# Kernel tuning notes

Measured on AMD Instinct MI355X. Metric: run time of the kernel, lower is better.

Reference implementation:

```python
import jax, jax.numpy as jnp
import numpy as np

B, S, D, H = 2, 2048, 1024, 16
DH = D // H

def setup_inputs() -> dict:
    key = jax.random.key(0)
    ks = jax.random.split(key, 8)
    scale = 0.02
    return {
        'query': jax.random.normal(ks[0], (B, S, D), jnp.float32),
        'key': jax.random.normal(ks[1], (B, S, D), jnp.float32),
        'value': jax.random.normal(ks[2], (B, S, D), jnp.float32),
        'mask': jax.random.randint(ks[3], (B, 1, 1, S), 0, 2).astype(jnp.float32),
        'Wq': jax.random.normal(ks[4], (D, D), jnp.float32) * scale,
        'bq': jnp.zeros((D,), jnp.float32),
        'Wk': jax.random.normal(ks[5], (D, D), jnp.float32) * scale,
        'bk': jnp.zeros((D,), jnp.float32),
        'Wv': jax.random.normal(ks[6], (D, D), jnp.float32) * scale,
        'bv': jnp.zeros((D,), jnp.float32),
        'Wo': jax.random.normal(ks[7], (D, D), jnp.float32) * scale,
        'bo': jnp.zeros((D,), jnp.float32),
    }

def _split_heads(x):
    # [B, S, D] -> [B, H, S, DH]
    b, s, _ = x.shape
    return x.reshape(b, s, H, DH).transpose(0, 2, 1, 3)

def reference(query, key, value, mask, Wq, bq, Wk, bk, Wv, bv, Wo, bo):
    q = _split_heads(query @ Wq + bq)
    k = _split_heads(key @ Wk + bk)
    v = _split_heads(value @ Wv + bv)
    logits = jnp.einsum('bhqd,bhkd->bhqk', q, k) / jnp.sqrt(jnp.float32(DH))
    logits = logits + mask * (-1e9)  # mask==1 means masked out
    attn = jax.nn.softmax(logits, axis=-1)
    out = jnp.einsum('bhqk,bhkd->bhqd', attn, v)  # [B,H,S,DH]
    out = out.transpose(0, 2, 1, 3).reshape(query.shape[0], -1, D)
    return out @ Wo + bo
```

## Files before the change

### kernel.cpp

```cpp
#include <hip/hip_runtime.h>
#include <hip/hip_bf16.h>
#include <stdint.h>

using short8  = __attribute__((ext_vector_type(8))) short;
using f32x4   = __attribute__((ext_vector_type(4))) float;
using f32x16  = __attribute__((ext_vector_type(16))) float;

__device__ inline unsigned short f2bf(float f) {
    union { float f; unsigned int u; } v; v.f = f;
    unsigned int u = v.u;
    unsigned int r = (u + 0x7FFFu + ((u >> 16) & 1u)) >> 16;
    return (unsigned short)r;
}

__device__ inline unsigned short bfu(float f) {
    __hip_bfloat16 h = __float2bfloat16(f);
    union { __hip_bfloat16 h; unsigned short u; } c; c.h = h;
    return c.u;
}

__device__ inline float bf2f(unsigned short u) {
    union { unsigned int u; float f; } v; v.u = (unsigned int)u << 16;
    return v.f;
}

__device__ inline unsigned int bfpk(float lo, float hi) {
    return (unsigned int)bfu(lo) | ((unsigned int)bfu(hi) << 16);
}

__device__ inline f32x4 mfma16(short8 a, short8 b, f32x4 c) {
    return __builtin_amdgcn_mfma_f32_16x16x32_bf16(a, b, c, 0, 0, 0);
}
__device__ inline f32x16 mfma32(short8 a, short8 b, f32x16 c) {
    return __builtin_amdgcn_mfma_f32_32x32x16_bf16(a, b, c, 0, 0, 0);
}

__device__ inline void gld16(const void* g, void* l) {
    __builtin_amdgcn_global_load_lds(
        (const __attribute__((address_space(1))) unsigned int*)g,
        (__attribute__((address_space(3))) unsigned int*)l, 16, 0, 0);
}

#define SEQ 2048
#define DIM 1024
#define NH  16
#define DH  64
#define MROWS 4096
#define OHALF 4194304
#define LHALF 65536

__global__ __launch_bounds__(256) void wcvt_kernel(
    const float* __restrict__ W0, const float* __restrict__ W1,
    const float* __restrict__ W2, const float* __restrict__ W3,
    unsigned short* __restrict__ Wt)
{
    __shared__ unsigned short tile[64][72];
    const float* W = (blockIdx.y == 0) ? W0 : (blockIdx.y == 1) ? W1
                   : (blockIdx.y == 2) ? W2 : W3;
    unsigned short* out = Wt + (size_t)blockIdx.y * DIM * DIM;
    const int t  = threadIdx.x;
    const int tk = blockIdx.x >> 4, tn = blockIdx.x & 15;
    const int k0 = tk * 64, n0 = tn * 64;

    #pragma unroll
    for (int j = 0; j < 4; ++j) {
        int c = t + j * 256;
        int r = c >> 4, c4 = c & 15;
        float4 v = *(const float4*)(W + (size_t)(k0 + r) * DIM + n0 + c4 * 4);
        tile[c4 * 4 + 0][r] = f2bf(v.x);
        tile[c4 * 4 + 1][r] = f2bf(v.y);
        tile[c4 * 4 + 2][r] = f2bf(v.z);
        tile[c4 * 4 + 3][r] = f2bf(v.w);
    }
    __syncthreads();
    #pragma unroll
    for (int j = 0; j < 2; ++j) {
        int c = t + j * 256;
        int r = c >> 3, c8 = c & 7;
        *(short8*)(out + (size_t)(n0 + r) * DIM + k0 + c8 * 8) =
            *(const short8*)&tile[r][c8 * 8];
    }
}

__global__ __launch_bounds__(256) void xcvt_kernel(
    const float* __restrict__ Xq, const float* __restrict__ Xk,
    const float* __restrict__ Xv, unsigned short* __restrict__ Xbf)
{
    const int zz = blockIdx.y;
    const float* src = (zz == 0) ? Xq : (zz == 1) ? Xk : Xv;
    size_t i8 = ((size_t)blockIdx.x * 256 + threadIdx.x) * 8;
    float4 v0 = *(const float4*)(src + i8);
    float4 v1 = *(const float4*)(src + i8 + 4);
    union { unsigned int u[4]; short8 s8; } p;
    p.u[0] = bfpk(v0.x, v0.y); p.u[1] = bfpk(v0.z, v0.w);
    p.u[2] = bfpk(v1.x, v1.y); p.u[3] = bfpk(v1.z, v1.w);
    *(short8*)(Xbf + (size_t)zz * MROWS * DIM + i8) = p.s8;
}

template<bool BF16A>
__global__ __launch_bounds__(256, 3) void proj_kernel(
    const unsigned short* __restrict__ Xbf,
    const float* __restrict__ Xq, const float* __restrict__ Xk, const float* __restrict__ Xv,
    const unsigned short* __restrict__ Wt,
    const float* __restrict__ bq, const float* __restrict__ bk, const float* __restrict__ bv,
    const float* __restrict__ maskp,
    unsigned short* __restrict__ Qh, unsigned short* __restrict__ Kh,
    unsigned short* __restrict__ Vt)
{
    __shared__ unsigned short Al[128][64];
    __shared__ unsigned short Bl[128][64];

    const int bid = blockIdx.x;
    const int z = bid >> 8;
    const int p = bid & 255;
    const int qq = p >> 3;
    const int mb = (p & 7) | ((qq & 3) << 3);
    const int nb = qq >> 2;
    const int m0 = mb * 128, n0 = nb * 128;

    const unsigned short* W = Wt + (size_t)z * DIM * DIM;
    const float* bias = (z == 0) ? bq : (z == 1) ? bk : bv;

    const int t = threadIdx.x, lane = t & 63, w = t >> 6;
    const int l16 = lane & 15, hi = lane >> 4;
    const int wm = w >> 1, wn = w & 1;
    const int row2 = t >> 1, part = t & 1;
    const int swz = (row2 & 7) << 3;
    const int cb = part * 32;

    const unsigned short* Asrc_bf = nullptr;
    const float* Asrc_f = nullptr;
    if constexpr (BF16A) {
        Asrc_bf = Xbf + (size_t)z * MROWS * DIM + (size_t)(m0 + row2) * DIM + cb;
    } else {
        const float* X = (z == 0) ? Xq : (z == 1) ? Xk : Xv;
        Asrc_f = X + (size_t)(m0 + row2) * DIM + cb;
    }
    const unsigned short* Bsrc = W + (size_t)(n0 + row2) * DIM + cb;

    f32x4 zero4 = {0.f, 0.f, 0.f, 0.f};
    f32x4 acc[4][4];
    #pragma unroll
    for (int i = 0; i < 4; ++i)
        #pragma unroll
        for (int j = 0; j < 4; ++j) acc[i][j] = zero4;

    short8 na[4], nbv[4];
    #pragma unroll
    for (int i = 0; i < 4; ++i) {
        if constexpr (BF16A) {
            na[i] = *(const short8*)(Asrc_bf + i * 8);
        } else {
            float4 f0 = *(const float4*)(Asrc_f + i * 8);
            float4 f1 = *(const float4*)(Asrc_f + i * 8 + 4);
            union { unsigned int u[4]; short8 s8; } pk;
            pk.u[0] = bfpk(f0.x, f0.y); pk.u[1] = bfpk(f0.z, f0.w);
            pk.u[2] = bfpk(f1.x, f1.y); pk.u[3] = bfpk(f1.z, f1.w);
            na[i] = pk.s8;
        }
        nbv[i] = *(const short8*)(Bsrc + i * 8);
    }
    #pragma unroll
    for (int i = 0; i < 4; ++i) {
        *(short8*)&Al[row2][(cb + i * 8) ^ swz] = na[i];
        *(short8*)&Bl[row2][(cb + i * 8) ^ swz] = nbv[i];
    }
    __syncthreads();

    for (int kt = 0; kt < DIM / 64; ++kt) {
        if (kt < DIM / 64 - 1) {
            const int k0n = (kt + 1) * 64;
            #pragma unroll
            for (int i = 0; i < 4; ++i) {
                if constexpr (BF16A) {
                    na[i] = *(const short8*)(Asrc_bf + k0n + i * 8);
                } else {
                    float4 f0 = *(const float4*)(Asrc_f + k0n + i * 8);
                    float4 f1 = *(const float4*)(Asrc_f + k0n + i * 8 + 4);
                    union { unsigned int u[4]; short8 s8; } pk;
                    pk.u[0] = bfpk(f0.x, f0.y); pk.u[1] = bfpk(f0.z, f0.w);
                    pk.u[2] = bfpk(f1.x, f1.y); pk.u[3] = bfpk(f1.z, f1.w);
                    na[i] = pk.s8;
                }
                nbv[i] = *(const short8*)(Bsrc + k0n + i * 8);
            }
        }
        #pragma unroll
        for (int kc = 0; kc < 2; ++kc) {
            short8 af[4], bfv[4];
            #pragma unroll
            for (int i = 0; i < 4; ++i) {
                int ra = wm * 64 + i * 16 + l16;
                af[i] = *(const short8*)&Al[ra][(kc * 32 + hi * 8) ^ ((ra & 7) << 3)];
            }
            #pragma unroll
            for (int j = 0; j < 4; ++j) {
                int rb = wn * 64 + j * 16 + l16;
                bfv[j] = *(const short8*)&Bl[rb][(kc * 32 + hi * 8) ^ ((rb & 7) << 3)];
            }
            #pragma unroll
            for (int i = 0; i < 4; ++i)
                #pragma unroll
                for (int j = 0; j < 4; ++j)
                    acc[i][j] = mfma16(af[i], bfv[j], acc[i][j]);
        }
        __syncthreads();
        if (kt < DIM / 64 - 1) {
            #pragma unroll
            for (int i = 0; i < 4; ++i) {
                *(short8*)&Al[row2][(cb + i * 8) ^ swz] = na[i];
                *(short8*)&Bl[row2][(cb + i * 8) ^ swz] = nbv[i];
            }
        }
        __syncthreads();
    }

    float bj[4];
    #pragma unroll
    for (int j = 0; j < 4; ++j) bj[j] = bias[n0 + wn * 64 + j * 16 + l16];

    if (z == 2) {
        #pragma unroll
        for (int i = 0; i < 4; ++i) {
            int mrow0 = m0 + wm * 64 + i * 16 + hi * 4;
            int bb = mrow0 >> 11, s = mrow0 & (SEQ - 1);
            float4 mv = *(const float4*)(maskp + (size_t)bb * SEQ + s);
            float w0 = 1.f - mv.x, w1 = 1.f - mv.y, w2 = 1.f - mv.z, w3 = 1.f - mv.w;
            #pragma unroll
            for (int j = 0; j < 4; ++j) {
                int n = n0 + wn * 64 + j * 16 + l16;
                int dn = n & 63, hh = n >> 6;
                ushort4 pk;
                pk.x = bfu((acc[i][j][0] + bj[j]) * w0);
                pk.y = bfu((acc[i][j][1] + bj[j]) * w1);
                pk.z = bfu((acc[i][j][2] + bj[j]) * w2);
                pk.w = bfu((acc[i][j][3] + bj[j]) * w3);
                int scol = (s & ~31) | ((((s >> 3) & 3) ^ ((dn >> 1) & 3)) << 3) | (s & 7);
                *(ushort4*)(Vt + ((size_t)(bb * NH + hh) * DH + dn) * SEQ + scol) = pk;
            }
        }
    } else if (z == 1) {
        #pragma unroll
        for (int i = 0; i < 4; ++i) {
            #pragma unroll
            for (int j = 0; j < 4; ++j) {
                int n = n0 + wn * 64 + j * 16 + l16;
                int hh = n >> 6, d = n & 63;
                #pragma unroll
                for (int r = 0; r < 4; ++r) {
                    int mrow = m0 + wm * 64 + i * 16 + hi * 4 + r;
                    int bb = mrow >> 11, s = mrow & (SEQ - 1);
                    int dsw = (d & 7) | ((((d >> 3) ^ (s & 7)) & 7) << 3);
                    Kh[((size_t)(bb * NH + hh) * SEQ + s) * DH + dsw] =
                        bfu(acc[i][j][r] + bj[j]);
                }
            }
        }
    } else {
        const float sc = 0.125f * 1.4426950408889634f;
        #pragma unroll
        for (int i = 0; i < 4; ++i) {
            #pragma unroll
            for (int j = 0; j < 4; ++j) {
                int n = n0 + wn * 64 + j * 16 + l16;
                int hh = n >> 6, d = n & 63;
                #pragma unroll
                for (int r = 0; r < 4; ++r) {
                    int mrow = m0 + wm * 64 + i * 16 + hi * 4 + r;
                    int bb = mrow >> 11, s = mrow & (SEQ - 1);
                    Qh[((size_t)(bb * NH + hh) * SEQ + s) * DH + d] =
                        bfu((acc[i][j][r] + bj[j]) * sc);
                }
            }
        }
    }
}

template<bool SPLIT>
__global__ __launch_bounds__(512) void attn_kernel(
    const unsigned short* __restrict__ Qh,
    const unsigned short* __restrict__ Kh,
    const unsigned short* __restrict__ Vtp,
    const float* __restrict__ mask,
    unsigned short* __restrict__ AO,
    unsigned short* __restrict__ Opart,
    float* __restrict__ lpart)
{
    constexpr int NT = SPLIT ? 32 : 64;
    __shared__ unsigned short Kl[2][32 * 64];
    __shared__ unsigned short Vl[2][64 * 32];
    __shared__ unsigned short Ml[2048];

    const int t = threadIdx.x, lane = t & 63, w = t >> 6;
    const int l31 = lane & 31, h32 = lane >> 5;
    const int bh = blockIdx.x, b = bh >> 4, h = bh & (NH - 1);
    const int q0 = blockIdx.y * 256 + w * 32;
    const int half = SPLIT ? blockIdx.z : 0;
    const int tile0 = half * NT;

    const unsigned short* Q = Qh + (size_t)bh * SEQ * DH;
    const unsigned short* K = Kh + (size_t)bh * SEQ * DH;
    const unsigned short* V = Vtp + (size_t)bh * DH * SEQ;

    const int cs = (w & 3) * 64 + lane;
    const bool isK = (w < 4);

    short8 qf[4];
    #pragma unroll
    for (int ds = 0; ds < 4; ++ds)
        qf[ds] = *(const short8*)(Q + (size_t)(q0 + l31) * DH + ds * 16 + h32 * 8);

    f32x16 o[2], ol;
    #pragma unroll
    for (int r = 0; r < 16; ++r) { o[0][r] = 0.f; o[1][r] = 0.f; ol[r] = 0.f; }

    {
        const int kb0 = tile0 * 32;
        if (isK) gld16(K + (size_t)(kb0 + (cs >> 3)) * DH + (cs & 7) * 8, &Kl[0][cs * 8]);
        else     gld16(V + (size_t)(cs >> 2) * SEQ + kb0 + (cs & 3) * 8,  &Vl[0][cs * 8]);
        const float* mb = mask + (size_t)b * SEQ + t * 4;
        float4 m = *(const float4*)mb;
        unsigned int pm0 = bfpk(1.f - m.x, 1.f - m.y);
        unsigned int pm1 = bfpk(1.f - m.z, 1.f - m.w);
        *(unsigned int*)&Ml[t * 4]     = pm0;
        *(unsigned int*)&Ml[t * 4 + 2] = pm1;
    }
    asm volatile("s_waitcnt vmcnt(0)" ::: "memory");
    __syncthreads();

    for (int it = 0; it < NT; ++it) {
        const int tile = tile0 + it;
        const int cur = it & 1;
        const int kb = tile * 32;
        const int nkb = ((tile + 1) & 63) * 32;

        if (isK) gld16(K + (size_t)(nkb + (cs >> 3)) * DH + (cs & 7) * 8, &Kl[cur ^ 1][cs * 8]);
        else     gld16(V + (size_t)(cs >> 2) * SEQ + nkb + (cs & 3) * 8,  &Vl[cur ^ 1][cs * 8]);

        short8 wf[2];
        #pragma unroll
        for (int ss = 0; ss < 2; ++ss)
            wf[ss] = *(const short8*)&Ml[kb + ss * 16 + h32 * 8];

        f32x16 st;
        #pragma unroll
        for (int r = 0; r < 16; ++r) st[r] = 0.f;
        __builtin_amdgcn_s_setprio(1);
        #pragma unroll
        for (int ds = 0; ds < 4; ++ds) {
            short8 kfr = *(const short8*)
                &Kl[cur][l31 * 64 + (((ds * 2 + h32) ^ (l31 & 7)) * 8)];
            st = mfma32(kfr, qf[ds], st);
        }
        __builtin_amdgcn_s_setprio(0);

        #pragma unroll
        for (int r = 0; r < 16; ++r) st[r] = exp2f(st[r]);

        short8 pa[2];
        #pragma unroll
        for (int ss = 0; ss < 2; ++ss) {
            const int rb = ss * 8;
            unsigned int a0 = bfpk(st[rb + 0], st[rb + 1]);
            unsigned int a1 = bfpk(st[rb + 2], st[rb + 3]);
            unsigned int b0 = bfpk(st[rb + 4], st[rb + 5]);
            unsigned int b1 = bfpk(st[rb + 6], st[rb + 7]);
            asm volatile("v_permlane32_swap_b32 %0, %1" : "+v"(a0), "+v"(b0));
            asm volatile("v_permlane32_swap_b32 %0, %1" : "+v"(a1), "+v"(b1));
            union { unsigned int u[4]; short8 s8; } up;
            up.u[0] = a0; up.u[1] = a1; up.u[2] = b0; up.u[3] = b1;
            pa[ss] = up.s8;
        }

        __builtin_amdgcn_s_setprio(1);
        #pragma unroll
        for (int ss = 0; ss < 2; ++ss) {
            #pragma unroll
            for (int dblk = 0; dblk < 2; ++dblk) {
                int vrow = dblk * 32 + l31;
                short8 vfr = *(const short8*)
                    &Vl[cur][vrow * 32 + (((ss * 2 + h32) ^ ((l31 >> 1) & 3)) * 8)];
                o[dblk] = mfma32(pa[ss], vfr, o[dblk]);
            }
            ol = mfma32(pa[ss], wf[ss], ol);
        }
        __builtin_amdgcn_s_setprio(0);

        asm volatile("s_waitcnt vmcnt(0)" ::: "memory");
        __syncthreads();
    }

    if constexpr (SPLIT) {
        #pragma unroll
        for (int dblk = 0; dblk < 2; ++dblk) {
            #pragma unroll
            for (int r = 0; r < 16; ++r) {
                int q = (r & 3) + 8 * (r >> 2) + 4 * h32;
                Opart[(size_t)half * OHALF + (size_t)(b * SEQ + q0 + q) * DIM
                      + h * DH + dblk * 32 + l31] = bfu(o[dblk][r]);
            }
        }
        if (l31 == 0) {
            #pragma unroll
            for (int r = 0; r < 16; ++r) {
                int q = (r & 3) + 8 * (r >> 2) + 4 * h32;
                lpart[(size_t)half * LHALF + bh * SEQ + q0 + q] = ol[r];
            }
        }
    } else {
        float rcl[16];
        #pragma unroll
        for (int r = 0; r < 16; ++r) rcl[r] = 1.0f / ol[r];
        #pragma unroll
        for (int dblk = 0; dblk < 2; ++dblk) {
            #pragma unroll
            for (int r = 0; r < 16; ++r) {
                int q = (r & 3) + 8 * (r >> 2) + 4 * h32;
                AO[(size_t)(b * SEQ + q0 + q) * DIM + h * DH + dblk * 32 + l31] =
                    bfu(o[dblk][r] * rcl[r]);
            }
        }
    }
}

template<bool SPLIT>
__global__ __launch_bounds__(256, 3) void outproj_kernel(
    const unsigned short* __restrict__ Op0, const float* __restrict__ lpart,
    const unsigned short* __restrict__ W,
    const float* __restrict__ bias, float* __restrict__ Out)
{
    __shared__ unsigned short Al[128][64];
    __shared__ unsigned short Bl[64][64];

    const int p = blockIdx.x;
    const int qq = p >> 3;
    const int mb = (p & 7) | ((qq & 3) << 3);
    const int nb = qq >> 2;
    const int m0 = mb * 128, n0 = nb * 64;

    const int t = threadIdx.x, lane = t & 63, w = t >> 6;
    const int l16 = lane & 15, hi = lane >> 4;
    const int wm = w >> 1, wn = w & 1;
    const int row2 = t >> 1, part = t & 1;
    const int swzA = (row2 & 7) << 3;
    const int cb = part * 32;
    const int row4 = t >> 2, part4 = t & 3;
    const int swzB = (row4 & 7) << 3;
    const int cb4 = part4 * 16;

    const int arow = m0 + row2;
    const int bb = arow >> 11, sA = arow & (SEQ - 1);
    const unsigned short* Asrc = Op0 + (size_t)arow * DIM + cb;
    const unsigned short* Bsrc = W + (size_t)(n0 + row4) * DIM + cb4;

    f32x4 zero4 = {0.f, 0.f, 0.f, 0.f};
    f32x4 acc[4][2];
    #pragma unroll
    for (int i = 0; i < 4; ++i) { acc[i][0] = zero4; acc[i][1] = zero4; }

    short8 o0[4], o1[4], nbv[2];
    float rlv = 0.f;

    auto load_kt = [&](int kt) {
        const int k0 = kt * 64;
        if constexpr (SPLIT) {
            size_t li = (size_t)(bb * NH + kt) * SEQ + sA;
            rlv = 1.0f / (lpart[li] + lpart[(size_t)LHALF + li]);
            #pragma unroll
            for (int i = 0; i < 4; ++i) {
                o0[i] = *(const short8*)(Asrc + k0 + i * 8);
                o1[i] = *(const short8*)(Asrc + (size_t)OHALF + k0 + i * 8);
            }
        } else {
            #pragma unroll
            for (int i = 0; i < 4; ++i)
                o0[i] = *(const short8*)(Asrc + k0 + i * 8);
        }
        #pragma unroll
        for (int c = 0; c < 2; ++c)
            nbv[c] = *(const short8*)(Bsrc + k0 + c * 8);
    };
    auto stage = [&]() {
        #pragma unroll
        for (int i = 0; i < 4; ++i) {
            short8 na;
            if constexpr (SPLIT) {
                union { unsigned int u[4]; short8 s8; } pk;
                #pragma unroll
                for (int j = 0; j < 4; ++j) {
                    float f0 = (bf2f((unsigned short)o0[i][2*j])   + bf2f((unsigned short)o1[i][2*j]))   * rlv;
                    float f1 = (bf2f((unsigned short)o0[i][2*j+1]) + bf2f((unsigned short)o1[i][2*j+1])) * rlv;
                    pk.u[j] = bfpk(f0, f1);
                }
                na = pk.s8;
            } else {
                na = o0[i];
            }
            *(short8*)&Al[row2][(cb + i * 8) ^ swzA] = na;
        }
        #pragma unroll
        for (int c = 0; c < 2; ++c)
            *(short8*)&Bl[row4][(cb4 + c * 8) ^ swzB] = nbv[c];
    };

    load_kt(0);
    stage();
    __syncthreads();

    for (int kt = 0; kt < DIM / 64; ++kt) {
        if (kt < DIM / 64 - 1) load_kt(kt + 1);
        #pragma unroll
        for (int kc = 0; kc < 2; ++kc) {
            short8 af[4], bfv[2];
            #pragma unroll
            for (int i = 0; i < 4; ++i) {
                int ra = wm * 64 + i * 16 + l16;
                af[i] = *(const short8*)&Al[ra][(kc * 32 + hi * 8) ^ ((ra & 7) << 3)];
            }
            #pragma unroll
            for (int j = 0; j < 2; ++j) {
                int rb = wn * 32 + j * 16 + l16;
                bfv[j] = *(const short8*)&Bl[rb][(kc * 32 + hi * 8) ^ ((rb & 7) << 3)];
            }
            #pragma unroll
            for (int i = 0; i < 4; ++i)
                #pragma unroll
                for (int j = 0; j < 2; ++j)
                    acc[i][j] = mfma16(af[i], bfv[j], acc[i][j]);
        }
        __syncthreads();
        if (kt < DIM / 64 - 1) {
            stage();
        }
        __syncthreads();
    }

    float bj[2];
    #pragma unroll
    for (int j = 0; j < 2; ++j) bj[j] = bias[n0 + wn * 32 + j * 16 + l16];
    #pragma unroll
    for (int i = 0; i < 4; ++i) {
        #pragma unroll
        for (int j = 0; j < 2; ++j) {
            int n = n0 + wn * 32 + j * 16 + l16;
            #pragma unroll
            for (int r = 0; r < 4; ++r) {
                int m = m0 + wm * 64 + i * 16 + hi * 4 + r;
                Out[(size_t)m * DIM + n] = acc[i][j][r] + bj[j];
            }
        }
    }
}

extern "C" void kernel_launch(void* const* d_in, const int* in_sizes, int n_in,
                              void* d_out, int out_size, void* d_ws, size_t ws_size,
                              hipStream_t stream) {
    const float* query = (const float*)d_in[0];
    const float* key   = (const float*)d_in[1];
    const float* value = (const float*)d_in[2];
    const float* mask  = (const float*)d_in[3];
    const float* Wq    = (const float*)d_in[4];
    const float* bq    = (const float*)d_in[5];
    const float* Wk    = (const float*)d_in[6];
    const float* bk    = (const float*)d_in[7];
    const float* Wv    = (const float*)d_in[8];
    const float* bv    = (const float*)d_in[9];
    const float* Wo    = (const float*)d_in[10];
    const float* bo    = (const float*)d_in[11];
    float* out = (float*)d_out;

    char* ws = (char*)d_ws;
    unsigned short* Wt    = (unsigned short*)(ws);
    unsigned short* Qh    = (unsigned short*)(ws + (size_t)8  * 1024 * 1024);
    unsigned short* Kh    = (unsigned short*)(ws + (size_t)16 * 1024 * 1024);
    unsigned short* Vt    = (unsigned short*)(ws + (size_t)24 * 1024 * 1024);
    unsigned short* Opart = (unsigned short*)(ws + (size_t)32 * 1024 * 1024);
    float*          lpart = (float*)         (ws + (size_t)48 * 1024 * 1024);
    unsigned short* Xbf   = (unsigned short*)(ws + (size_t)32 * 1024 * 1024);
    const unsigned short* WtO = Wt + (size_t)3 * 1024 * 1024;

    wcvt_kernel<<<dim3(256, 4), 256, 0, stream>>>(Wq, Wk, Wv, Wo, Wt);
    if (ws_size >= (size_t)56 * 1024 * 1024) {
        xcvt_kernel<<<dim3(2048, 3), 256, 0, stream>>>(query, key, value, Xbf);
        proj_kernel<true><<<768, 256, 0, stream>>>(Xbf, query, key, value, Wt,
                                                   bq, bk, bv, mask, Qh, Kh, Vt);
        attn_kernel<true><<<dim3(32, 8, 2), 512, 0, stream>>>(Qh, Kh, Vt, mask,
                                                              nullptr, Opart, lpart);
        outproj_kernel<true><<<512, 256, 0, stream>>>(Opart, lpart, WtO, bo, out);
    } else {
        proj_kernel<false><<<768, 256, 0, stream>>>(nullptr, query, key, value, Wt,
                                                    bq, bk, bv, mask, Qh, Kh, Vt);
        attn_kernel<false><<<dim3(32, 8, 1), 512, 0, stream>>>(Qh, Kh, Vt, mask,
                                                               Opart, nullptr, nullptr);
        outproj_kernel<false><<<512, 256, 0, stream>>>(Opart, nullptr, WtO, bo, out);
    }
}
```

Measured before the change: 144.7 us.

## Compact unmasked keys/values so attention only iterates over valid key tiles

```diff
diff --git a/kernel.cpp b/kernel.cpp
--- a/kernel.cpp
+++ b/kernel.cpp
@@ -80,6 +80,48 @@
         *(short8*)(out + (size_t)(n0 + r) * DIM + k0 + c8 * 8) =
             *(const short8*)&tile[r][c8 * 8];
     }
+}
+
+__global__ __launch_bounds__(256) void mask_scan_kernel(
+    const float* __restrict__ mask, int* __restrict__ pos, int* __restrict__ cnt)
+{
+    __shared__ int sums[256];
+    const int b = blockIdx.x, t = threadIdx.x;
+    const float* m = mask + (size_t)b * SEQ;
+    int flags[8], s = 0;
+    #pragma unroll
+    for (int i = 0; i < 8; ++i) {
+        flags[i] = (m[t * 8 + i] == 0.0f) ? 1 : 0;
+        s += flags[i];
+    }
+    sums[t] = s;
+    __syncthreads();
+    if (t == 0) {
+        int acc = 0;
+        for (int i = 0; i < 256; ++i) { int x = sums[i]; sums[i] = acc; acc += x; }
+        cnt[b] = acc;
+    }
+    __syncthreads();
+    int base = sums[t];
+    #pragma unroll
+    for (int i = 0; i < 8; ++i) {
+        pos[(size_t)b * SEQ + t * 8 + i] = flags[i] ? base : -1;
+        base += flags[i];
+    }
+}
+
+__global__ __launch_bounds__(256) void pad_kernel(
+    const int* __restrict__ cnt, unsigned short* __restrict__ Kh,
+    unsigned short* __restrict__ Vt)
+{
+    const int bh = blockIdx.x, b = bh >> 4;
+    const int c = cnt[b];
+    if ((c & 31) == 0) return;
+    const int base = c & ~31;
+    const int t = threadIdx.x;
+    short8 z = {0, 0, 0, 0, 0, 0, 0, 0};
+    *(short8*)(Kh + ((size_t)bh * SEQ + base + (t >> 3)) * DH + (t & 7) * 8) = z;
+    *(short8*)(Vt + (size_t)bh * DH * SEQ + (size_t)(t >> 2) * SEQ + base + (t & 3) * 8) = z;
 }
 
 __global__ __launch_bounds__(256) void xcvt_kernel(
@@ -103,7 +145,7 @@
     const float* __restrict__ Xq, const float* __restrict__ Xk, const float* __restrict__ Xv,
     const unsigned short* __restrict__ Wt,
     const float* __restrict__ bq, const float* __restrict__ bk, const float* __restrict__ bv,
-    const float* __restrict__ maskp,
+    const int* __restrict__ pos,
     unsigned short* __restrict__ Qh, unsigned short* __restrict__ Kh,
     unsigned short* __restrict__ Vt)
 {
@@ -224,34 +266,36 @@
         for (int i = 0; i < 4; ++i) {
             int mrow0 = m0 + wm * 64 + i * 16 + hi * 4;
             int bb = mrow0 >> 11, s = mrow0 & (SEQ - 1);
-            float4 mv = *(const float4*)(maskp + (size_t)bb * SEQ + s);
-            float w0 = 1.f - mv.x, w1 = 1.f - mv.y, w2 = 1.f - mv.z, w3 = 1.f - mv.w;
-            #pragma unroll
-            for (int j = 0; j < 4; ++j) {
-                int n = n0 + wn * 64 + j * 16 + l16;
-                int dn = n & 63, hh = n >> 6;
-                ushort4 pk;
-                pk.x = bfu((acc[i][j][0] + bj[j]) * w0);
-                pk.y = bfu((acc[i][j][1] + bj[j]) * w1);
-                pk.z = bfu((acc[i][j][2] + bj[j]) * w2);
-                pk.w = bfu((acc[i][j][3] + bj[j]) * w3);
-                int scol = (s & ~31) | ((((s >> 3) & 3) ^ ((dn >> 1) & 3)) << 3) | (s & 7);
-                *(ushort4*)(Vt + ((size_t)(bb * NH + hh) * DH + dn) * SEQ + scol) = pk;
+            #pragma unroll
+            for (int r = 0; r < 4; ++r) {
+                int p_ = pos[(size_t)bb * SEQ + s + r];
+                if (p_ < 0) continue;
+                #pragma unroll
+                for (int j = 0; j < 4; ++j) {
+                    int n = n0 + wn * 64 + j * 16 + l16;
+                    int dn = n & 63, hh = n >> 6;
+                    int scol = (p_ & ~31) | ((((p_ >> 3) & 3) ^ ((dn >> 1) & 3)) << 3)
+                             | (p_ & 7);
+                    Vt[((size_t)(bb * NH + hh) * DH + dn) * SEQ + scol] =
+                        bfu(acc[i][j][r] + bj[j]);
+                }
             }
         }
     } else if (z == 1) {
         #pragma unroll
         for (int i = 0; i < 4; ++i) {
-            #pragma unroll
-            for (int j = 0; j < 4; ++j) {
-                int n = n0 + wn * 64 + j * 16 + l16;
-                int hh = n >> 6, d = n & 63;
-                #pragma unroll
-                for (int r = 0; r < 4; ++r) {
-                    int mrow = m0 + wm * 64 + i * 16 + hi * 4 + r;
-                    int bb = mrow >> 11, s = mrow & (SEQ - 1);
-                    int dsw = (d & 7) | ((((d >> 3) ^ (s & 7)) & 7) << 3);
-                    Kh[((size_t)(bb * NH + hh) * SEQ + s) * DH + dsw] =
+            int mrow0 = m0 + wm * 64 + i * 16 + hi * 4;
+            int bb = mrow0 >> 11, s = mrow0 & (SEQ - 1);
+            #pragma unroll
+            for (int r = 0; r < 4; ++r) {
+                int p_ = pos[(size_t)bb * SEQ + s + r];
+                if (p_ < 0) continue;
+                #pragma unroll
+                for (int j = 0; j < 4; ++j) {
+                    int n = n0 + wn * 64 + j * 16 + l16;
+                    int hh = n >> 6, d = n & 63;
+                    int dsw = (d & 7) | ((((d >> 3) ^ (p_ & 7)) & 7) << 3);
+                    Kh[((size_t)(bb * NH + hh) * SEQ + p_) * DH + dsw] =
                         bfu(acc[i][j][r] + bj[j]);
                 }
             }
@@ -281,22 +325,25 @@
     const unsigned short* __restrict__ Qh,
     const unsigned short* __restrict__ Kh,
     const unsigned short* __restrict__ Vtp,
-    const float* __restrict__ mask,
+    const int* __restrict__ cntbuf,
     unsigned short* __restrict__ AO,
     unsigned short* __restrict__ Opart,
     float* __restrict__ lpart)
 {
-    constexpr int NT = SPLIT ? 32 : 64;
     __shared__ unsigned short Kl[2][32 * 64];
     __shared__ unsigned short Vl[2][64 * 32];
-    __shared__ unsigned short Ml[2048];
 
     const int t = threadIdx.x, lane = t & 63, w = t >> 6;
     const int l31 = lane & 31, h32 = lane >> 5;
     const int bh = blockIdx.x, b = bh >> 4, h = bh & (NH - 1);
     const int q0 = blockIdx.y * 256 + w * 32;
     const int half = SPLIT ? blockIdx.z : 0;
-    const int tile0 = half * NT;
+
+    const int cnt = cntbuf[b];
+    const int NTt = (cnt + 31) >> 5;
+    const int NTh0 = (NTt + 1) >> 1;
+    const int t0   = (SPLIT && half) ? NTh0 : 0;
+    const int myNT = SPLIT ? (half ? NTt - NTh0 : NTh0) : NTt;
 
     const unsigned short* Q = Qh + (size_t)bh * SEQ * DH;
     const unsigned short* K = Kh + (size_t)bh * SEQ * DH;
@@ -315,32 +362,36 @@
     for (int r = 0; r < 16; ++r) { o[0][r] = 0.f; o[1][r] = 0.f; ol[r] = 0.f; }
 
     {
-        const int kb0 = tile0 * 32;
+        const int kb0 = t0 * 32;
         if (isK) gld16(K + (size_t)(kb0 + (cs >> 3)) * DH + (cs & 7) * 8, &Kl[0][cs * 8]);
         else     gld16(V + (size_t)(cs >> 2) * SEQ + kb0 + (cs & 3) * 8,  &Vl[0][cs * 8]);
-        const float* mb = mask + (size_t)b * SEQ + t * 4;
-        float4 m = *(const float4*)mb;
-        unsigned int pm0 = bfpk(1.f - m.x, 1.f - m.y);
-        unsigned int pm1 = bfpk(1.f - m.z, 1.f - m.w);
-        *(unsigned int*)&Ml[t * 4]     = pm0;
-        *(unsigned int*)&Ml[t * 4 + 2] = pm1;
     }
     asm volatile("s_waitcnt vmcnt(0)" ::: "memory");
     __syncthreads();
 
-    for (int it = 0; it < NT; ++it) {
-        const int tile = tile0 + it;
+    for (int it = 0; it < myNT; ++it) {
+        const int tile = t0 + it;
         const int cur = it & 1;
         const int kb = tile * 32;
-        const int nkb = ((tile + 1) & 63) * 32;
+        const int nt_ = (it + 1 < myNT) ? (tile + 1) : t0;
+        const int nkb = nt_ * 32;
 
         if (isK) gld16(K + (size_t)(nkb + (cs >> 3)) * DH + (cs & 7) * 8, &Kl[cur ^ 1][cs * 8]);
         else     gld16(V + (size_t)(cs >> 2) * SEQ + nkb + (cs & 3) * 8,  &Vl[cur ^ 1][cs * 8]);
 
         short8 wf[2];
-        #pragma unroll
-        for (int ss = 0; ss < 2; ++ss)
-            wf[ss] = *(const short8*)&Ml[kb + ss * 16 + h32 * 8];
+        if (kb + 32 <= cnt) {
+            #pragma unroll
+            for (int ss = 0; ss < 2; ++ss)
+                #pragma unroll
+                for (int e = 0; e < 8; ++e) wf[ss][e] = (short)0x3F80;
+        } else {
+            #pragma unroll
+            for (int ss = 0; ss < 2; ++ss)
+                #pragma unroll
+                for (int e = 0; e < 8; ++e)
+                    wf[ss][e] = (short)((kb + ss * 16 + h32 * 8 + e < cnt) ? 0x3F80 : 0);
+        }
 
         f32x16 st;
         #pragma unroll
@@ -389,6 +440,7 @@
         asm volatile("s_waitcnt vmcnt(0)" ::: "memory");
         __syncthreads();
     }
+    asm volatile("s_waitcnt vmcnt(0)" ::: "memory");
 
     if constexpr (SPLIT) {
         #pragma unroll
@@ -577,20 +629,24 @@
     unsigned short* Opart = (unsigned short*)(ws + (size_t)32 * 1024 * 1024);
     float*          lpart = (float*)         (ws + (size_t)48 * 1024 * 1024);
     unsigned short* Xbf   = (unsigned short*)(ws + (size_t)32 * 1024 * 1024);
+    int* pos  = (int*)d_out;
+    int* cntb = (int*)d_out + 2 * SEQ;
     const unsigned short* WtO = Wt + (size_t)3 * 1024 * 1024;
 
     wcvt_kernel<<<dim3(256, 4), 256, 0, stream>>>(Wq, Wk, Wv, Wo, Wt);
+    mask_scan_kernel<<<2, 256, 0, stream>>>(mask, pos, cntb);
+    pad_kernel<<<32, 256, 0, stream>>>(cntb, Kh, Vt);
     if (ws_size >= (size_t)56 * 1024 * 1024) {
         xcvt_kernel<<<dim3(2048, 3), 256, 0, stream>>>(query, key, value, Xbf);
         proj_kernel<true><<<768, 256, 0, stream>>>(Xbf, query, key, value, Wt,
-                                                   bq, bk, bv, mask, Qh, Kh, Vt);
-        attn_kernel<true><<<dim3(32, 8, 2), 512, 0, stream>>>(Qh, Kh, Vt, mask,
+                                                   bq, bk, bv, pos, Qh, Kh, Vt);
+        attn_kernel<true><<<dim3(32, 8, 2), 512, 0, stream>>>(Qh, Kh, Vt, cntb,
                                                               nullptr, Opart, lpart);
         outproj_kernel<true><<<512, 256, 0, stream>>>(Opart, lpart, WtO, bo, out);
     } else {
         proj_kernel<false><<<768, 256, 0, stream>>>(nullptr, query, key, value, Wt,
-                                                    bq, bk, bv, mask, Qh, Kh, Vt);
-        attn_kernel<false><<<dim3(32, 8, 1), 512, 0, stream>>>(Qh, Kh, Vt, mask,
+                                                    bq, bk, bv, pos, Qh, Kh, Vt);
+        attn_kernel<false><<<dim3(32, 8, 1), 512, 0, stream>>>(Qh, Kh, Vt, cntb,
                                                                Opart, nullptr, nullptr);
         outproj_kernel<false><<<512, 256, 0, stream>>>(Opart, nullptr, WtO, bo, out);
     }
```

Measured after the change: 133.4 us. 1.08x faster.
